# Kernel optimization log

Measured on AMD Instinct MI355X. Metric: run time of the kernel, lower is better.

## Reference

```python
import jax, jax.numpy as jnp
import numpy as np

A = 0.2            # leak rate
SIG_IN = 0.05      # sigma_input_noise
SIG_REC = 0.05     # sigma_rec_noise
N = 256            # n_right_neurons (configs['n_neurons']); left hemi has 2 neurons


def setup_inputs() -> dict:
    key = jax.random.key(0)
    ks = jax.random.split(key, 9)
    B, T = 512, 400

    def nrm(k, shape, scale=1.0):
        return jax.random.normal(k, shape, dtype=jnp.float32) * scale

    xs = nrm(ks[0], (B, T, 2))
    # recurrent weights (asymmetric init, matching torch init_params)
    w_ll = nrm(ks[1], (2, 2), 1.0 / np.sqrt(2))
    b_ll = jnp.zeros((2,), jnp.float32)
    w_rr = nrm(ks[2], (N, N), 1.0 / np.sqrt(N))
    w_rr = w_rr * (3.6 / jnp.sum(jnp.abs(w_rr)))
    b_rr = jnp.zeros((N,), jnp.float32)
    w_lr = nrm(ks[3], (N, 2), 1.0 / np.sqrt(N + 2))   # left -> right
    w_rl = nrm(ks[4], (2, N), 1.0 / np.sqrt(N + 2))   # right -> left
    # input projections (one_hot=True: 2 input channels)
    w_xl = nrm(ks[5], (2, 2))
    w_xr = nrm(ks[6], (N, 2))
    # readout (N+2 -> 1), rescaled so sum(|w|)=3.0
    w_ro = nrm(ks[7], (1, N + 2), 1.0 / np.sqrt(N))
    w_ro = w_ro * (3.0 / jnp.sum(jnp.abs(w_ro)))
    b_ro = jnp.zeros((1,), jnp.float32)
    return {"xs": xs, "w_ll": w_ll, "b_ll": b_ll, "w_rr": w_rr, "b_rr": b_rr,
            "w_lr": w_lr, "w_rl": w_rl, "w_xl": w_xl, "w_xr": w_xr,
            "w_ro": w_ro, "b_ro": b_ro}


def reference(xs, w_ll, b_ll, w_rr, b_rr, w_lr, w_rl, w_xl, w_xr, w_ro, b_ro):
    B, T, _ = xs.shape
    scale = np.sqrt(2.0 / A)
    nk = jax.random.split(jax.random.key(42), 3)
    # input noise (drop masks are all-ones since drop_p=0, amps = 1.0)
    noise_l = scale * SIG_IN * jax.random.normal(nk[0], xs.shape, xs.dtype)
    noise_r = scale * SIG_IN * jax.random.normal(nk[1], xs.shape, xs.dtype)
    x_l = (xs + noise_l) @ w_xl.T                      # (B,T,2)
    x_r = (xs + noise_r) @ w_xr.T                      # (B,T,N)
    x_inj = jnp.concatenate([x_l, x_r], axis=-1)       # (B,T,N+2)
    # recurrent noise, pregenerated for the scan
    rec_noise = scale * SIG_REC * jax.random.normal(nk[2], (T, B, N + 2), xs.dtype)

    def step(h, inp):
        x_t, nz = inp
        hl, hr = h[:, :2], h[:, 2:]
        left = hl @ w_ll.T + hr @ w_rl.T + b_ll        # (B,2)
        right = hl @ w_lr.T + hr @ w_rr.T + b_rr       # (B,N)
        pre = jnp.concatenate([left, right], axis=1) + x_t + nz
        h_new = (1.0 - A) * h + A * jnp.tanh(pre)
        return h_new, h_new

    h0 = jnp.zeros((B, N + 2), xs.dtype)
    _, hs = jax.lax.scan(step, h0, (jnp.swapaxes(x_inj, 0, 1), rec_noise))
    hs = jnp.swapaxes(hs, 0, 1)                        # (B,T,N+2)
    zs = hs @ w_ro.T + b_ro                            # (B,T,1)
    return hs, zs
```

## Files before the change

kernel.cpp:

```cpp
#include <hip/hip_runtime.h>
#include <stdint.h>
#include <stddef.h>


typedef uint32_t u32x4 __attribute__((ext_vector_type(4)));
typedef __fp16   f16x2 __attribute__((ext_vector_type(2)));

#define TF_ROUND(x0, x1, r) { x0 += x1; x1 = ((x1) << (r)) | ((x1) >> (32 - (r))); x1 ^= x0; }

__host__ __device__ inline void tf2x32(uint32_t k0, uint32_t k1, uint32_t x0, uint32_t x1,
                                       uint32_t& o0, uint32_t& o1) {
  uint32_t ks2 = k0 ^ k1 ^ 0x1BD11BDAu;
  x0 += k0; x1 += k1;
  TF_ROUND(x0, x1, 13) TF_ROUND(x0, x1, 15) TF_ROUND(x0, x1, 26) TF_ROUND(x0, x1, 6)
  x0 += k1; x1 += ks2 + 1u;
  TF_ROUND(x0, x1, 17) TF_ROUND(x0, x1, 29) TF_ROUND(x0, x1, 16) TF_ROUND(x0, x1, 24)
  x0 += ks2; x1 += k0 + 2u;
  TF_ROUND(x0, x1, 13) TF_ROUND(x0, x1, 15) TF_ROUND(x0, x1, 26) TF_ROUND(x0, x1, 6)
  x0 += k0; x1 += k1 + 3u;
  TF_ROUND(x0, x1, 17) TF_ROUND(x0, x1, 29) TF_ROUND(x0, x1, 16) TF_ROUND(x0, x1, 24)
  x0 += k1; x1 += ks2 + 4u;
  TF_ROUND(x0, x1, 13) TF_ROUND(x0, x1, 15) TF_ROUND(x0, x1, 26) TF_ROUND(x0, x1, 6)
  x0 += ks2; x1 += k0 + 5u;
  o0 = x0; o1 = x1;
}

__device__ __forceinline__ float jax_erfinv(float x) {
  float w = -log1pf(-x * x);
  float p;
  if (w < 5.0f) {
    w -= 2.5f;
    p = 2.81022636e-08f;
    p = fmaf(p, w, 3.43273939e-07f);
    p = fmaf(p, w, -3.5233877e-06f);
    p = fmaf(p, w, -4.39150654e-06f);
    p = fmaf(p, w, 0.00021858087f);
    p = fmaf(p, w, -0.00125372503f);
    p = fmaf(p, w, -0.00417768164f);
    p = fmaf(p, w, 0.246640727f);
    p = fmaf(p, w, 1.50140941f);
  } else {
    w = sqrtf(w) - 3.0f;
    p = -0.000200214257f;
    p = fmaf(p, w, 0.000100950558f);
    p = fmaf(p, w, 0.00134934322f);
    p = fmaf(p, w, -0.00367342844f);
    p = fmaf(p, w, 0.00573950773f);
    p = fmaf(p, w, -0.0076224613f);
    p = fmaf(p, w, 0.00943887047f);
    p = fmaf(p, w, 1.00167406f);
    p = fmaf(p, w, 2.83297682f);
  }
  return p * x;
}

__device__ __forceinline__ float uni_from_bits(uint32_t bits) {
  float f = __uint_as_float((bits >> 9) | 0x3f800000u) - 1.0f;
  float x = f * 2.0f + (-0.99999994f);
  return fmaxf(-0.99999994f, x);
}

__device__ __forceinline__ float noise_from_bits(uint32_t bits) {
  float n = 1.41421356f * jax_erfinv(uni_from_bits(bits));
  return 0.15811388f * n;
}

__device__ __forceinline__ float my_tanh(float x) {
  float e = __expf(2.0f * x);
  return 1.0f - 2.0f / (e + 1.0f);
}

__device__ __forceinline__ uint32_t packh2(float a, float b) {
  f16x2 h = __builtin_amdgcn_cvt_pkrtz(a, b);
  return __builtin_bit_cast(uint32_t, h);
}

__device__ __forceinline__ void pkfma(uint32_t& acc, uint32_t w, uint32_t h) {
  asm("v_pk_fma_f16 %0, %1, %2, %0" : "+v"(acc) : "v"(w), "v"(h));
}

__device__ __forceinline__ float cvt2f(uint32_t a) {
  f16x2 v = __builtin_bit_cast(f16x2, a);
  return (float)v.x + (float)v.y;
}

__device__ __forceinline__ void step_barrier() {
  asm volatile("s_waitcnt lgkmcnt(0)" ::: "memory");
  __builtin_amdgcn_s_barrier();
}

__device__ __forceinline__ float allred8(float x) {
  int t = __builtin_amdgcn_update_dpp(0, __float_as_int(x), 0xB1, 0xF, 0xF, true);
  x += __int_as_float(t);
  t = __builtin_amdgcn_update_dpp(0, __float_as_int(x), 0x4E, 0xF, 0xF, true);
  x += __int_as_float(t);
  t = __builtin_amdgcn_ds_swizzle(__float_as_int(x), 0x101F);
  x += __int_as_float(t);
  return x;
}

#define PK(kp) (20 * ((kp) >> 4) + ((kp) & 15))

__device__ __forceinline__ float wval(int j, int k,
    const float* w_ll, const float* w_rl, const float* w_lr, const float* w_rr) {
  if (j < 2) return (k < 2) ? w_ll[j * 2 + k] : w_rl[j * 256 + (k - 2)];
  return (k < 2) ? w_lr[(j - 2) * 2 + k] : w_rr[(j - 2) * 256 + (k - 2)];
}

__global__ __launch_bounds__(256) void build_w_kernel(
    const float* __restrict__ w_ll, const float* __restrict__ w_rl,
    const float* __restrict__ w_lr, const float* __restrict__ w_rr,
    uint32_t* __restrict__ Wp, float* __restrict__ Wtail) {
  int i = blockIdx.x * 256 + threadIdx.x;
  if (i < 258 * 128) {
    int j = i >> 7, kp = i & 127;
    float v0 = wval(j, 2 * kp, w_ll, w_rl, w_lr, w_rr);
    float v1 = wval(j, 2 * kp + 1, w_ll, w_rl, w_lr, w_rr);
    Wp[i] = packh2(v0, v1);
  }
  if (i < 516) {
    int j = i >> 1, k = 256 + (i & 1);
    Wtail[i] = wval(j, k, w_ll, w_rl, w_lr, w_rr);
  }
}

__global__ __launch_bounds__(256) void gen_uv_kernel(
    const float* __restrict__ xs, float* __restrict__ u, float* __restrict__ v,
    uint32_t k0a, uint32_t k0b, uint32_t k1a, uint32_t k1b) {
  uint32_t i = blockIdx.x * 256u + threadIdx.x;
  bool isv = i >= 409600u;
  uint32_t e = isv ? i - 409600u : i;
  uint32_t ka = isv ? k1a : k0a;
  uint32_t kb = isv ? k1b : k0b;
  uint32_t o0, o1;
  tf2x32(ka, kb, 0u, e, o0, o1);
  float val = xs[e] + noise_from_bits(o0 ^ o1);
  if (isv) v[e] = val; else u[e] = val;
}

__global__ __launch_bounds__(256) void gen_c_kernel(
    const float* __restrict__ u, const float* __restrict__ v,
    const float* __restrict__ w_xl, const float* __restrict__ w_xr,
    const float* __restrict__ b_ll, const float* __restrict__ b_rr,
    float* __restrict__ C, uint32_t ka, uint32_t kb) {
  uint32_t i = blockIdx.x * 256u + threadIdx.x;
  uint32_t t = i / 132096u;
  uint32_t rem = i - t * 132096u;
  uint32_t b = rem / 258u;
  uint32_t j = rem - b * 258u;
  uint32_t o0, o1;
  tf2x32(ka, kb, 0u, i, o0, o1);
  float nz = noise_from_bits(o0 ^ o1);
  uint32_t bt = (b * 400u + t) * 2u;
  float inj;
  if (j < 2u) {
    float2 uu = *(const float2*)(u + bt);
    inj = w_xl[j * 2u] * uu.x + w_xl[j * 2u + 1u] * uu.y + b_ll[j];
  } else {
    uint32_t jr = j - 2u;
    float2 vv = *(const float2*)(v + bt);
    inj = w_xr[jr * 2u] * vv.x + w_xr[jr * 2u + 1u] * vv.y + b_rr[jr];
  }
  C[(size_t)(b * 400u + t) * 258u + j] = inj + nz;
}

__global__ __launch_bounds__(512, 4) void rnn_scan_kernel(
    const uint32_t* __restrict__ Wp, const float* __restrict__ Wtail,
    float* __restrict__ hsC, const float* __restrict__ w_ro,
    const float* __restrict__ b_ro) {
  __shared__ __align__(16) uint32_t hbp[2][168];
  __shared__ __align__(16) uint32_t wlp[2][168];
  __shared__ __align__(16) float cbuf[8][260];
  __shared__ __align__(16) float sbuf[8][260];
  __shared__ __align__(16) float wrol[260];

  const int tid = threadIdx.x;
  const int ks = tid & 7;
  const int g  = tid >> 3;
  const int j0 = 2 + 4 * g;

  u32x4 wv[4][4];
  float2 wt[4];
#pragma unroll
  for (int r = 0; r < 4; ++r) {
    const uint32_t* p = Wp + (j0 + r) * 128 + 16 * ks;
#pragma unroll
    for (int c = 0; c < 4; ++c) wv[r][c] = *(const u32x4*)(p + 4 * c);
    wt[r] = *(const float2*)(Wtail + (j0 + r) * 2);
  }
  const float bro = b_ro[0];

  if (tid < 256) {
    int row = tid >> 7, kp = tid & 127;
    wlp[row][PK(kp)] = Wp[row * 128 + kp];
  }
  if (tid < 4) {
    int row = tid >> 1;
    wlp[row][160 + (tid & 1)] = __float_as_uint(Wtail[row * 2 + (tid & 1)]);
  }
  if (tid < 258) {
    int jj = (tid < 2) ? (256 + tid) : (tid - 2);
    wrol[jj] = w_ro[tid];
  }
  for (int idx = tid; idx < 336; idx += 512) ((uint32_t*)hbp)[idx] = 0u;

  const float* gC = hsC + (size_t)blockIdx.x * 103200;
  float* gO       = hsC + (size_t)blockIdx.x * 103200;
  float* gZ       = hsC + (size_t)52838400 + (size_t)blockIdx.x * 400;

  for (int idx = tid; idx < 2064; idx += 512) {
    int s = idx / 258, j = idx - 258 * s;
    int jj = (j < 2) ? (256 + j) : (j - 2);
    cbuf[s][jj] = gC[idx];
  }
  __syncthreads();

  float hcur[4] = {0.f, 0.f, 0.f, 0.f};
  float hL0 = 0.f, hL1 = 0.f;

#pragma unroll 1
  for (int cc = 0; cc < 50; ++cc) {
    float creg[5];
    const bool hn = (cc < 49);
    const int nb = (cc + 1) * 2064;
    if (hn) {
#pragma unroll
      for (int q = 0; q < 5; ++q) {
        int idx = tid + 512 * q;
        if (idx < 2064) creg[q] = gC[nb + idx];
      }
    }

#pragma unroll
    for (int s = 0; s < 8; ++s) {
      const int cur = s & 1, nxt = cur ^ 1;

      uint32_t ac0 = 0u, ac1 = 0u, ac2 = 0u, ac3 = 0u;
#pragma unroll
      for (int c = 0; c < 4; ++c) {
        u32x4 hq = *(const u32x4*)&hbp[cur][20 * ks + 4 * c];
        u32x4 w0 = wv[0][c], w1 = wv[1][c], w2 = wv[2][c], w3 = wv[3][c];
        pkfma(ac0, w0.x, hq.x); pkfma(ac0, w0.y, hq.y);
        pkfma(ac0, w0.z, hq.z); pkfma(ac0, w0.w, hq.w);
        pkfma(ac1, w1.x, hq.x); pkfma(ac1, w1.y, hq.y);
        pkfma(ac1, w1.z, hq.z); pkfma(ac1, w1.w, hq.w);
        pkfma(ac2, w2.x, hq.x); pkfma(ac2, w2.y, hq.y);
        pkfma(ac2, w2.z, hq.z); pkfma(ac2, w2.w, hq.w);
        pkfma(ac3, w3.x, hq.x); pkfma(ac3, w3.y, hq.y);
        pkfma(ac3, w3.z, hq.z); pkfma(ac3, w3.w, hq.w);
      }
      float a0 = cvt2f(ac0);
      float a1 = cvt2f(ac1);
      float a2 = cvt2f(ac2);
      float a3 = cvt2f(ac3);

      float l0 = 0.f, l1 = 0.f;
      if (tid < 8) {
        uint32_t lc0 = 0u, lc1 = 0u;
#pragma unroll
        for (int c = 0; c < 4; ++c) {
          u32x4 hq = *(const u32x4*)&hbp[cur][20 * tid + 4 * c];
          u32x4 w0 = *(const u32x4*)&wlp[0][20 * tid + 4 * c];
          u32x4 w1 = *(const u32x4*)&wlp[1][20 * tid + 4 * c];
          pkfma(lc0, w0.x, hq.x); pkfma(lc0, w0.y, hq.y);
          pkfma(lc0, w0.z, hq.z); pkfma(lc0, w0.w, hq.w);
          pkfma(lc1, w1.x, hq.x); pkfma(lc1, w1.y, hq.y);
          pkfma(lc1, w1.z, hq.z); pkfma(lc1, w1.w, hq.w);
        }
        l0 = allred8(cvt2f(lc0));
        l1 = allred8(cvt2f(lc1));
      }

      a0 = allred8(a0); a1 = allred8(a1); a2 = allred8(a2); a3 = allred8(a3);

      const float t0 = __uint_as_float(hbp[cur][160]);
      const float t1 = __uint_as_float(hbp[cur][161]);

      if (ks == 0) {
        float4 cv = *(const float4*)&cbuf[s][4 * g];
        float pre0 = a0 + wt[0].x * t0 + wt[0].y * t1 + cv.x;
        float pre1 = a1 + wt[1].x * t0 + wt[1].y * t1 + cv.y;
        float pre2 = a2 + wt[2].x * t0 + wt[2].y * t1 + cv.z;
        float pre3 = a3 + wt[3].x * t0 + wt[3].y * t1 + cv.w;
        hcur[0] = 0.8f * hcur[0] + 0.2f * my_tanh(pre0);
        hcur[1] = 0.8f * hcur[1] + 0.2f * my_tanh(pre1);
        hcur[2] = 0.8f * hcur[2] + 0.2f * my_tanh(pre2);
        hcur[3] = 0.8f * hcur[3] + 0.2f * my_tanh(pre3);
        uint32_t p01 = packh2(hcur[0], hcur[1]);
        uint32_t p23 = packh2(hcur[2], hcur[3]);
        if (g == 63) {
          hbp[nxt][PK(127)] = p01;
          hbp[nxt][160] = __float_as_uint(hcur[2]);
          hbp[nxt][161] = __float_as_uint(hcur[3]);
        } else {
          hbp[nxt][PK(1 + 2 * g)] = p01;
          hbp[nxt][PK(2 + 2 * g)] = p23;
        }
        *(float4*)&sbuf[s][4 * g] = make_float4(hcur[0], hcur[1], hcur[2], hcur[3]);
      }

      if (tid == 0) {
        float wl0t0 = __uint_as_float(wlp[0][160]);
        float wl0t1 = __uint_as_float(wlp[0][161]);
        float wl1t0 = __uint_as_float(wlp[1][160]);
        float wl1t1 = __uint_as_float(wlp[1][161]);
        float pre0 = l0 + wl0t0 * t0 + wl0t1 * t1 + cbuf[s][256];
        float pre1 = l1 + wl1t0 * t0 + wl1t1 * t1 + cbuf[s][257];
        hL0 = 0.8f * hL0 + 0.2f * my_tanh(pre0);
        hL1 = 0.8f * hL1 + 0.2f * my_tanh(pre1);
        hbp[nxt][0] = packh2(hL0, hL1);
        sbuf[s][256] = hL0;
        sbuf[s][257] = hL1;
      }

      step_barrier();
    }

    const int fb = cc * 2064;
    for (int idx = tid; idx < 2064; idx += 512) {
      int s = idx / 258, j = idx - 258 * s;
      int jj = (j < 2) ? (256 + j) : (j - 2);
      gO[fb + idx] = sbuf[s][jj];
    }

    {
      int w = tid >> 6, lane = tid & 63;
      float zacc = 0.f;
#pragma unroll
      for (int q = 0; q < 5; ++q) {
        int jj = lane + 64 * q;
        if (jj < 258) zacc = fmaf(sbuf[w][jj], wrol[jj], zacc);
      }
#pragma unroll
      for (int m = 32; m >= 1; m >>= 1) zacc += __shfl_xor(zacc, m);
      if (lane == 0) gZ[cc * 8 + w] = zacc + bro;
    }

    if (hn) {
#pragma unroll
      for (int q = 0; q < 5; ++q) {
        int idx = tid + 512 * q;
        if (idx < 2064) {
          int s = idx / 258, j = idx - 258 * s;
          int jj = (j < 2) ? (256 + j) : (j - 2);
          cbuf[s][jj] = creg[q];
        }
      }
    }
    step_barrier();
  }
}

extern "C" void kernel_launch(void* const* d_in, const int* in_sizes, int n_in,
                              void* d_out, int out_size, void* d_ws, size_t ws_size,
                              hipStream_t stream) {
  const float* xs   = (const float*)d_in[0];
  const float* w_ll = (const float*)d_in[1];
  const float* b_ll = (const float*)d_in[2];
  const float* w_rr = (const float*)d_in[3];
  const float* b_rr = (const float*)d_in[4];
  const float* w_lr = (const float*)d_in[5];
  const float* w_rl = (const float*)d_in[6];
  const float* w_xl = (const float*)d_in[7];
  const float* w_xr = (const float*)d_in[8];
  const float* w_ro = (const float*)d_in[9];
  const float* b_ro = (const float*)d_in[10];

  float* hs = (float*)d_out;

  uint32_t* Wp  = (uint32_t*)d_ws;
  float* Wtail  = (float*)(Wp + 33024);
  float* u      = Wtail + 516;
  float* v      = u + 409600;

  uint32_t nk[3][2];
  for (uint32_t i = 0; i < 3; ++i) {
    uint32_t o0, o1;
    tf2x32(0u, 42u, 0u, i, o0, o1);
    nk[i][0] = o0; nk[i][1] = o1;
  }

  build_w_kernel<<<129, 256, 0, stream>>>(w_ll, w_rl, w_lr, w_rr, Wp, Wtail);
  gen_uv_kernel<<<3200, 256, 0, stream>>>(xs, u, v, nk[0][0], nk[0][1], nk[1][0], nk[1][1]);
  gen_c_kernel<<<206400, 256, 0, stream>>>(u, v, w_xl, w_xr, b_ll, b_rr, hs, nk[2][0], nk[2][1]);
  rnn_scan_kernel<<<512, 512, 0, stream>>>(Wp, Wtail, hs, w_ro, b_ro);
}
```

Measured before the change: 1.021 ms.

## Fuse noise and input-injection generation into scan kernel and repartition matvec

Removes the separate gen_uv and gen_c kernels. Each scan block now generates its own input noise into shared memory once, then builds the next 8-step chunk of the drive term (threefry noise plus input projection) in place between chunks. This avoids writing and re-reading the full B*T*258 drive tensor through global memory. The recurrent matvec is also repartitioned: 4 lanes per output pair with 32-wide K slices, a 4-way DPP reduction, weights pinned in registers, and a compacted h buffer layout. The cost is that the threefry and erfinv arithmetic now sits on the serial scan's critical path between chunks, and register pressure goes up.

```diff
diff --git a/kernel.cpp b/kernel.cpp
--- a/kernel.cpp
+++ b/kernel.cpp
@@ -70,11 +70,6 @@
   return 1.0f - 2.0f / (e + 1.0f);
 }
 
-__device__ __forceinline__ uint32_t packh2(float a, float b) {
-  f16x2 h = __builtin_amdgcn_cvt_pkrtz(a, b);
-  return __builtin_bit_cast(uint32_t, h);
-}
-
 __device__ __forceinline__ void pkfma(uint32_t& acc, uint32_t w, uint32_t h) {
   asm("v_pk_fma_f16 %0, %1, %2, %0" : "+v"(acc) : "v"(w), "v"(h));
 }
@@ -84,27 +79,34 @@
   return (float)v.x + (float)v.y;
 }
 
+__device__ __forceinline__ u32x4 pin4(u32x4 x) { asm("" : "+v"(x)); return x; }
+__device__ __forceinline__ float2 pin2(float2 x) { asm("" : "+v"(x)); return x; }
+
 __device__ __forceinline__ void step_barrier() {
   asm volatile("s_waitcnt lgkmcnt(0)" ::: "memory");
   __builtin_amdgcn_s_barrier();
 }
 
-__device__ __forceinline__ float allred8(float x) {
+__device__ __forceinline__ float allred4(float x) {
   int t = __builtin_amdgcn_update_dpp(0, __float_as_int(x), 0xB1, 0xF, 0xF, true);
   x += __int_as_float(t);
   t = __builtin_amdgcn_update_dpp(0, __float_as_int(x), 0x4E, 0xF, 0xF, true);
   x += __int_as_float(t);
-  t = __builtin_amdgcn_ds_swizzle(__float_as_int(x), 0x101F);
-  x += __int_as_float(t);
   return x;
 }
 
-#define PK(kp) (20 * ((kp) >> 4) + ((kp) & 15))
+#define PKQ(acc, wq, hq) { pkfma(acc, (wq).x, (hq).x); pkfma(acc, (wq).y, (hq).y); \
+                           pkfma(acc, (wq).z, (hq).z); pkfma(acc, (wq).w, (hq).w); }
 
 __device__ __forceinline__ float wval(int j, int k,
     const float* w_ll, const float* w_rl, const float* w_lr, const float* w_rr) {
   if (j < 2) return (k < 2) ? w_ll[j * 2 + k] : w_rl[j * 256 + (k - 2)];
   return (k < 2) ? w_lr[(j - 2) * 2 + k] : w_rr[(j - 2) * 256 + (k - 2)];
+}
+
+__device__ __forceinline__ uint32_t packh2(float a, float b) {
+  f16x2 h = __builtin_amdgcn_cvt_pkrtz(a, b);
+  return __builtin_bit_cast(uint32_t, h);
 }
 
 __global__ __launch_bounds__(256) void build_w_kernel(
@@ -124,203 +126,180 @@
   }
 }
 
-__global__ __launch_bounds__(256) void gen_uv_kernel(
-    const float* __restrict__ xs, float* __restrict__ u, float* __restrict__ v,
-    uint32_t k0a, uint32_t k0b, uint32_t k1a, uint32_t k1b) {
-  uint32_t i = blockIdx.x * 256u + threadIdx.x;
-  bool isv = i >= 409600u;
-  uint32_t e = isv ? i - 409600u : i;
-  uint32_t ka = isv ? k1a : k0a;
-  uint32_t kb = isv ? k1b : k0b;
-  uint32_t o0, o1;
-  tf2x32(ka, kb, 0u, e, o0, o1);
-  float val = xs[e] + noise_from_bits(o0 ^ o1);
-  if (isv) v[e] = val; else u[e] = val;
-}
-
-__global__ __launch_bounds__(256) void gen_c_kernel(
-    const float* __restrict__ u, const float* __restrict__ v,
+__global__ __launch_bounds__(512, 4) void rnn_scan_kernel(
+    const uint32_t* __restrict__ Wp, const float* __restrict__ Wtail,
+    float* __restrict__ hsC,
+    const float* __restrict__ w_ro, const float* __restrict__ b_ro,
+    const float* __restrict__ xs,
     const float* __restrict__ w_xl, const float* __restrict__ w_xr,
     const float* __restrict__ b_ll, const float* __restrict__ b_rr,
-    float* __restrict__ C, uint32_t ka, uint32_t kb) {
-  uint32_t i = blockIdx.x * 256u + threadIdx.x;
-  uint32_t t = i / 132096u;
-  uint32_t rem = i - t * 132096u;
-  uint32_t b = rem / 258u;
-  uint32_t j = rem - b * 258u;
-  uint32_t o0, o1;
-  tf2x32(ka, kb, 0u, i, o0, o1);
-  float nz = noise_from_bits(o0 ^ o1);
-  uint32_t bt = (b * 400u + t) * 2u;
-  float inj;
-  if (j < 2u) {
-    float2 uu = *(const float2*)(u + bt);
-    inj = w_xl[j * 2u] * uu.x + w_xl[j * 2u + 1u] * uu.y + b_ll[j];
-  } else {
-    uint32_t jr = j - 2u;
-    float2 vv = *(const float2*)(v + bt);
-    inj = w_xr[jr * 2u] * vv.x + w_xr[jr * 2u + 1u] * vv.y + b_rr[jr];
-  }
-  C[(size_t)(b * 400u + t) * 258u + j] = inj + nz;
-}
-
-__global__ __launch_bounds__(512, 4) void rnn_scan_kernel(
-    const uint32_t* __restrict__ Wp, const float* __restrict__ Wtail,
-    float* __restrict__ hsC, const float* __restrict__ w_ro,
-    const float* __restrict__ b_ro) {
-  __shared__ __align__(16) uint32_t hbp[2][168];
-  __shared__ __align__(16) uint32_t wlp[2][168];
+    uint32_t k0a, uint32_t k0b, uint32_t k1a, uint32_t k1b,
+    uint32_t k2a, uint32_t k2b) {
+  __shared__ __align__(16) uint32_t hbp[2][132];
+  __shared__ __align__(16) uint32_t wlp[2][132];
   __shared__ __align__(16) float cbuf[8][260];
   __shared__ __align__(16) float sbuf[8][260];
-  __shared__ __align__(16) float wrol[260];
+  __shared__ float wrol[260];
+  __shared__ float uvb[400][4];
+  __shared__ float wxr[256][2];
+  __shared__ float brr[256];
+  __shared__ float wxl[4];
+  __shared__ float bll[2];
 
   const int tid = threadIdx.x;
-  const int ks = tid & 7;
-  const int g  = tid >> 3;
-  const int j0 = 2 + 4 * g;
-
-  u32x4 wv[4][4];
-  float2 wt[4];
-#pragma unroll
-  for (int r = 0; r < 4; ++r) {
-    const uint32_t* p = Wp + (j0 + r) * 128 + 16 * ks;
-#pragma unroll
-    for (int c = 0; c < 4; ++c) wv[r][c] = *(const u32x4*)(p + 4 * c);
-    wt[r] = *(const float2*)(Wtail + (j0 + r) * 2);
-  }
+  const int brow = blockIdx.x;
+  const int ks = tid & 3;
+  const int g  = tid >> 2;
+  const int j0 = 2 + 2 * g;
+  const int lrow = (tid >= 4) ? 1 : 0;
+
+  u32x4 wr0[8], wr1[8];
+  {
+    const uint32_t* p0 = Wp + (size_t)j0 * 128 + 32 * ks;
+    const uint32_t* p1 = p0 + 128;
+#pragma unroll
+    for (int c = 0; c < 8; ++c) {
+      wr0[c] = pin4(*(const u32x4*)(p0 + 4 * c));
+      wr1[c] = pin4(*(const u32x4*)(p1 + 4 * c));
+    }
+  }
+  const float2 wt0 = pin2(*(const float2*)(Wtail + (size_t)j0 * 2));
+  const float2 wt1 = pin2(*(const float2*)(Wtail + (size_t)j0 * 2 + 2));
   const float bro = b_ro[0];
 
   if (tid < 256) {
+    wxr[tid][0] = w_xr[2 * tid];
+    wxr[tid][1] = w_xr[2 * tid + 1];
+    brr[tid] = b_rr[tid];
     int row = tid >> 7, kp = tid & 127;
-    wlp[row][PK(kp)] = Wp[row * 128 + kp];
-  }
-  if (tid < 4) {
-    int row = tid >> 1;
-    wlp[row][160 + (tid & 1)] = __float_as_uint(Wtail[row * 2 + (tid & 1)]);
-  }
-  if (tid < 258) {
-    int jj = (tid < 2) ? (256 + tid) : (tid - 2);
-    wrol[jj] = w_ro[tid];
-  }
-  for (int idx = tid; idx < 336; idx += 512) ((uint32_t*)hbp)[idx] = 0u;
-
-  const float* gC = hsC + (size_t)blockIdx.x * 103200;
-  float* gO       = hsC + (size_t)blockIdx.x * 103200;
-  float* gZ       = hsC + (size_t)52838400 + (size_t)blockIdx.x * 400;
-
-  for (int idx = tid; idx < 2064; idx += 512) {
-    int s = idx / 258, j = idx - 258 * s;
-    int jj = (j < 2) ? (256 + j) : (j - 2);
-    cbuf[s][jj] = gC[idx];
+    wlp[row][kp] = Wp[row * 128 + kp];
+  }
+  if (tid < 4) wxl[tid] = w_xl[tid];
+  if (tid < 2) bll[tid] = b_ll[tid];
+  if (tid < 4) { int row = tid >> 1; wlp[row][128 + (tid & 1)] = __float_as_uint(Wtail[row * 2 + (tid & 1)]); }
+  if (tid < 258) { int jj = (tid < 2) ? (256 + tid) : (tid - 2); wrol[jj] = w_ro[tid]; }
+  for (int i2 = tid; i2 < 264; i2 += 512) ((uint32_t*)hbp)[i2] = 0u;
+
+  for (int idx = tid; idx < 1600; idx += 512) {
+    int t = idx >> 2, q = idx & 3;
+    uint32_t e = (uint32_t)(brow * 800 + t * 2 + (q & 1));
+    uint32_t o0, o1;
+    if (q < 2) tf2x32(k0a, k0b, 0u, e, o0, o1);
+    else       tf2x32(k1a, k1b, 0u, e, o0, o1);
+    uvb[t][q] = xs[e] + noise_from_bits(o0 ^ o1);
   }
   __syncthreads();
 
-  float hcur[4] = {0.f, 0.f, 0.f, 0.f};
-  float hL0 = 0.f, hL1 = 0.f;
+  auto gen_cbuf = [&](int cc) {
+#pragma unroll
+    for (int q = 0; q < 5; ++q) {
+      int idx = tid + 512 * q;
+      if (idx < 2064) {
+        int s = idx / 258;
+        int j = idx - 258 * s;
+        int t = cc * 8 + s;
+        uint32_t o0, o1;
+        tf2x32(k2a, k2b, 0u, (uint32_t)(t * 132096 + brow * 258 + j), o0, o1);
+        float nz = noise_from_bits(o0 ^ o1);
+        float inj;
+        int jj;
+        if (j < 2) {
+          inj = wxl[2 * j] * uvb[t][0] + wxl[2 * j + 1] * uvb[t][1] + bll[j];
+          jj = 256 + j;
+        } else {
+          int jr = j - 2;
+          inj = wxr[jr][0] * uvb[t][2] + wxr[jr][1] * uvb[t][3] + brr[jr];
+          jj = jr;
+        }
+        cbuf[s][jj] = inj + nz;
+      }
+    }
+  };
+
+  gen_cbuf(0);
+  __syncthreads();
+
+  float hcur = 0.f;
+  float hL = 0.f;
+
+  float* gO = hsC + (size_t)brow * 103200;
+  float* gZ = hsC + (size_t)52838400 + (size_t)brow * 400;
 
 #pragma unroll 1
   for (int cc = 0; cc < 50; ++cc) {
-    float creg[5];
-    const bool hn = (cc < 49);
-    const int nb = (cc + 1) * 2064;
-    if (hn) {
-#pragma unroll
-      for (int q = 0; q < 5; ++q) {
-        int idx = tid + 512 * q;
-        if (idx < 2064) creg[q] = gC[nb + idx];
-      }
-    }
-
 #pragma unroll
     for (int s = 0; s < 8; ++s) {
       const int cur = s & 1, nxt = cur ^ 1;
 
-      uint32_t ac0 = 0u, ac1 = 0u, ac2 = 0u, ac3 = 0u;
-#pragma unroll
-      for (int c = 0; c < 4; ++c) {
-        u32x4 hq = *(const u32x4*)&hbp[cur][20 * ks + 4 * c];
-        u32x4 w0 = wv[0][c], w1 = wv[1][c], w2 = wv[2][c], w3 = wv[3][c];
-        pkfma(ac0, w0.x, hq.x); pkfma(ac0, w0.y, hq.y);
-        pkfma(ac0, w0.z, hq.z); pkfma(ac0, w0.w, hq.w);
-        pkfma(ac1, w1.x, hq.x); pkfma(ac1, w1.y, hq.y);
-        pkfma(ac1, w1.z, hq.z); pkfma(ac1, w1.w, hq.w);
-        pkfma(ac2, w2.x, hq.x); pkfma(ac2, w2.y, hq.y);
-        pkfma(ac2, w2.z, hq.z); pkfma(ac2, w2.w, hq.w);
-        pkfma(ac3, w3.x, hq.x); pkfma(ac3, w3.y, hq.y);
-        pkfma(ac3, w3.z, hq.z); pkfma(ac3, w3.w, hq.w);
-      }
-      float a0 = cvt2f(ac0);
-      float a1 = cvt2f(ac1);
-      float a2 = cvt2f(ac2);
-      float a3 = cvt2f(ac3);
-
-      float l0 = 0.f, l1 = 0.f;
+      float t0 = __uint_as_float(hbp[cur][128]);
+      float t1 = __uint_as_float(hbp[cur][129]);
+      float2 cv = *(const float2*)&cbuf[s][2 * g];
+
+      const uint32_t* hb = &hbp[cur][32 * ks];
+      uint32_t acA0 = 0u, acA1 = 0u, acB0 = 0u, acB1 = 0u, lcA = 0u, lcB = 0u;
+      {
+        u32x4 h0 = *(const u32x4*)(hb + 0),  h1 = *(const u32x4*)(hb + 4),
+              h2 = *(const u32x4*)(hb + 8),  h3 = *(const u32x4*)(hb + 12);
+        PKQ(acA0, wr0[0], h0) PKQ(acA0, wr0[1], h1) PKQ(acA0, wr0[2], h2) PKQ(acA0, wr0[3], h3)
+        PKQ(acA1, wr1[0], h0) PKQ(acA1, wr1[1], h1) PKQ(acA1, wr1[2], h2) PKQ(acA1, wr1[3], h3)
+        if (tid < 8) {
+          const uint32_t* wl = &wlp[lrow][32 * ks];
+          u32x4 w0 = *(const u32x4*)(wl + 0), w1 = *(const u32x4*)(wl + 4),
+                w2 = *(const u32x4*)(wl + 8), w3 = *(const u32x4*)(wl + 12);
+          PKQ(lcA, w0, h0) PKQ(lcA, w1, h1) PKQ(lcA, w2, h2) PKQ(lcA, w3, h3)
+        }
+      }
+      {
+        u32x4 h0 = *(const u32x4*)(hb + 16), h1 = *(const u32x4*)(hb + 20),
+              h2 = *(const u32x4*)(hb + 24), h3 = *(const u32x4*)(hb + 28);
+        PKQ(acB0, wr0[4], h0) PKQ(acB0, wr0[5], h1) PKQ(acB0, wr0[6], h2) PKQ(acB0, wr0[7], h3)
+        PKQ(acB1, wr1[4], h0) PKQ(acB1, wr1[5], h1) PKQ(acB1, wr1[6], h2) PKQ(acB1, wr1[7], h3)
+        if (tid < 8) {
+          const uint32_t* wl = &wlp[lrow][32 * ks + 16];
+          u32x4 w0 = *(const u32x4*)(wl + 0), w1 = *(const u32x4*)(wl + 4),
+                w2 = *(const u32x4*)(wl + 8), w3 = *(const u32x4*)(wl + 12);
+          PKQ(lcB, w0, h0) PKQ(lcB, w1, h1) PKQ(lcB, w2, h2) PKQ(lcB, w3, h3)
+        }
+      }
+
+      float a0 = allred4(cvt2f(acA0) + cvt2f(acB0));
+      float a1 = allred4(cvt2f(acA1) + cvt2f(acB1));
+
+      if (ks < 2) {
+        float a   = ks ? a1 : a0;
+        float2 wt = ks ? wt1 : wt0;
+        float cvx = ks ? cv.y : cv.x;
+        float pre = a + wt.x * t0 + wt.y * t1 + cvx;
+        hcur = 0.8f * hcur + 0.2f * my_tanh(pre);
+        sbuf[s][2 * g + ks] = hcur;
+        if (g == 127) hbp[nxt][128 + ks] = __float_as_uint(hcur);
+        else *(__fp16*)((char*)&hbp[nxt][0] + 4 * (1 + g) + 2 * ks) = (__fp16)hcur;
+      }
+
       if (tid < 8) {
-        uint32_t lc0 = 0u, lc1 = 0u;
-#pragma unroll
-        for (int c = 0; c < 4; ++c) {
-          u32x4 hq = *(const u32x4*)&hbp[cur][20 * tid + 4 * c];
-          u32x4 w0 = *(const u32x4*)&wlp[0][20 * tid + 4 * c];
-          u32x4 w1 = *(const u32x4*)&wlp[1][20 * tid + 4 * c];
-          pkfma(lc0, w0.x, hq.x); pkfma(lc0, w0.y, hq.y);
-          pkfma(lc0, w0.z, hq.z); pkfma(lc0, w0.w, hq.w);
-          pkfma(lc1, w1.x, hq.x); pkfma(lc1, w1.y, hq.y);
-          pkfma(lc1, w1.z, hq.z); pkfma(lc1, w1.w, hq.w);
+        float l = allred4(cvt2f(lcA) + cvt2f(lcB));
+        if ((tid & 3) == 0) {
+          float wlt0 = __uint_as_float(wlp[lrow][128]);
+          float wlt1 = __uint_as_float(wlp[lrow][129]);
+          float pre = l + wlt0 * t0 + wlt1 * t1 + cbuf[s][256 + lrow];
+          hL = 0.8f * hL + 0.2f * my_tanh(pre);
+          sbuf[s][256 + lrow] = hL;
+          *(__fp16*)((char*)&hbp[nxt][0] + 2 * lrow) = (__fp16)hL;
         }
-        l0 = allred8(cvt2f(lc0));
-        l1 = allred8(cvt2f(lc1));
-      }
-
-      a0 = allred8(a0); a1 = allred8(a1); a2 = allred8(a2); a3 = allred8(a3);
-
-      const float t0 = __uint_as_float(hbp[cur][160]);
-      const float t1 = __uint_as_float(hbp[cur][161]);
-
-      if (ks == 0) {
-        float4 cv = *(const float4*)&cbuf[s][4 * g];
-        float pre0 = a0 + wt[0].x * t0 + wt[0].y * t1 + cv.x;
-        float pre1 = a1 + wt[1].x * t0 + wt[1].y * t1 + cv.y;
-        float pre2 = a2 + wt[2].x * t0 + wt[2].y * t1 + cv.z;
-        float pre3 = a3 + wt[3].x * t0 + wt[3].y * t1 + cv.w;
-        hcur[0] = 0.8f * hcur[0] + 0.2f * my_tanh(pre0);
-        hcur[1] = 0.8f * hcur[1] + 0.2f * my_tanh(pre1);
-        hcur[2] = 0.8f * hcur[2] + 0.2f * my_tanh(pre2);
-        hcur[3] = 0.8f * hcur[3] + 0.2f * my_tanh(pre3);
-        uint32_t p01 = packh2(hcur[0], hcur[1]);
-        uint32_t p23 = packh2(hcur[2], hcur[3]);
-        if (g == 63) {
-          hbp[nxt][PK(127)] = p01;
-          hbp[nxt][160] = __float_as_uint(hcur[2]);
-          hbp[nxt][161] = __float_as_uint(hcur[3]);
-        } else {
-          hbp[nxt][PK(1 + 2 * g)] = p01;
-          hbp[nxt][PK(2 + 2 * g)] = p23;
-        }
-        *(float4*)&sbuf[s][4 * g] = make_float4(hcur[0], hcur[1], hcur[2], hcur[3]);
-      }
-
-      if (tid == 0) {
-        float wl0t0 = __uint_as_float(wlp[0][160]);
-        float wl0t1 = __uint_as_float(wlp[0][161]);
-        float wl1t0 = __uint_as_float(wlp[1][160]);
-        float wl1t1 = __uint_as_float(wlp[1][161]);
-        float pre0 = l0 + wl0t0 * t0 + wl0t1 * t1 + cbuf[s][256];
-        float pre1 = l1 + wl1t0 * t0 + wl1t1 * t1 + cbuf[s][257];
-        hL0 = 0.8f * hL0 + 0.2f * my_tanh(pre0);
-        hL1 = 0.8f * hL1 + 0.2f * my_tanh(pre1);
-        hbp[nxt][0] = packh2(hL0, hL1);
-        sbuf[s][256] = hL0;
-        sbuf[s][257] = hL1;
       }
 
       step_barrier();
     }
 
     const int fb = cc * 2064;
-    for (int idx = tid; idx < 2064; idx += 512) {
-      int s = idx / 258, j = idx - 258 * s;
-      int jj = (j < 2) ? (256 + j) : (j - 2);
-      gO[fb + idx] = sbuf[s][jj];
+#pragma unroll
+    for (int q = 0; q < 5; ++q) {
+      int idx = tid + 512 * q;
+      if (idx < 2064) {
+        int s = idx / 258, j = idx - 258 * s;
+        int jj = (j < 2) ? (256 + j) : (j - 2);
+        gO[fb + idx] = sbuf[s][jj];
+      }
     }
 
     {
@@ -336,17 +315,7 @@
       if (lane == 0) gZ[cc * 8 + w] = zacc + bro;
     }
 
-    if (hn) {
-#pragma unroll
-      for (int q = 0; q < 5; ++q) {
-        int idx = tid + 512 * q;
-        if (idx < 2064) {
-          int s = idx / 258, j = idx - 258 * s;
-          int jj = (j < 2) ? (256 + j) : (j - 2);
-          cbuf[s][jj] = creg[q];
-        }
-      }
-    }
+    if (cc < 49) gen_cbuf(cc + 1);
     step_barrier();
   }
 }
@@ -370,8 +339,6 @@
 
   uint32_t* Wp  = (uint32_t*)d_ws;
   float* Wtail  = (float*)(Wp + 33024);
-  float* u      = Wtail + 516;
-  float* v      = u + 409600;
 
   uint32_t nk[3][2];
   for (uint32_t i = 0; i < 3; ++i) {
@@ -381,7 +348,8 @@
   }
 
   build_w_kernel<<<129, 256, 0, stream>>>(w_ll, w_rl, w_lr, w_rr, Wp, Wtail);
-  gen_uv_kernel<<<3200, 256, 0, stream>>>(xs, u, v, nk[0][0], nk[0][1], nk[1][0], nk[1][1]);
-  gen_c_kernel<<<206400, 256, 0, stream>>>(u, v, w_xl, w_xr, b_ll, b_rr, hs, nk[2][0], nk[2][1]);
-  rnn_scan_kernel<<<512, 512, 0, stream>>>(Wp, Wtail, hs, w_ro, b_ro);
-}
+  rnn_scan_kernel<<<512, 512, 0, stream>>>(Wp, Wtail, hs, w_ro, b_ro, xs,
+                                           w_xl, w_xr, b_ll, b_rr,
+                                           nk[0][0], nk[0][1], nk[1][0], nk[1][1],
+                                           nk[2][0], nk[2][1]);
+}
```

New measurement: 1.557 ms. 1.52x slower.

## Fuse noise and input-injection generation into the RNN scan kernel

Applied to the files above, without the earlier changes.

Removes the separate gen_uv and gen_c kernels, so each scan block now generates its own threefry noise and input projection on chip, one 8-step chunk at a time, between chunks. This drops the full-size write and read of the injected-input tensor through global memory, along with two kernel launches. In exchange, the threefry hashing sits on the serial scan's critical path between chunks instead of overlapping with the global prefetch. Shared memory also grows to hold the per-row noisy inputs and the projection weights, and empty asm statements pin the weight registers.

```diff
diff --git a/kernel.cpp b/kernel.cpp
--- a/kernel.cpp
+++ b/kernel.cpp
@@ -124,57 +124,28 @@
   }
 }
 
-__global__ __launch_bounds__(256) void gen_uv_kernel(
-    const float* __restrict__ xs, float* __restrict__ u, float* __restrict__ v,
-    uint32_t k0a, uint32_t k0b, uint32_t k1a, uint32_t k1b) {
-  uint32_t i = blockIdx.x * 256u + threadIdx.x;
-  bool isv = i >= 409600u;
-  uint32_t e = isv ? i - 409600u : i;
-  uint32_t ka = isv ? k1a : k0a;
-  uint32_t kb = isv ? k1b : k0b;
-  uint32_t o0, o1;
-  tf2x32(ka, kb, 0u, e, o0, o1);
-  float val = xs[e] + noise_from_bits(o0 ^ o1);
-  if (isv) v[e] = val; else u[e] = val;
-}
-
-__global__ __launch_bounds__(256) void gen_c_kernel(
-    const float* __restrict__ u, const float* __restrict__ v,
+__global__ __launch_bounds__(512, 4) void rnn_scan_kernel(
+    const uint32_t* __restrict__ Wp, const float* __restrict__ Wtail,
+    float* __restrict__ hsC,
+    const float* __restrict__ w_ro, const float* __restrict__ b_ro,
+    const float* __restrict__ xs,
     const float* __restrict__ w_xl, const float* __restrict__ w_xr,
     const float* __restrict__ b_ll, const float* __restrict__ b_rr,
-    float* __restrict__ C, uint32_t ka, uint32_t kb) {
-  uint32_t i = blockIdx.x * 256u + threadIdx.x;
-  uint32_t t = i / 132096u;
-  uint32_t rem = i - t * 132096u;
-  uint32_t b = rem / 258u;
-  uint32_t j = rem - b * 258u;
-  uint32_t o0, o1;
-  tf2x32(ka, kb, 0u, i, o0, o1);
-  float nz = noise_from_bits(o0 ^ o1);
-  uint32_t bt = (b * 400u + t) * 2u;
-  float inj;
-  if (j < 2u) {
-    float2 uu = *(const float2*)(u + bt);
-    inj = w_xl[j * 2u] * uu.x + w_xl[j * 2u + 1u] * uu.y + b_ll[j];
-  } else {
-    uint32_t jr = j - 2u;
-    float2 vv = *(const float2*)(v + bt);
-    inj = w_xr[jr * 2u] * vv.x + w_xr[jr * 2u + 1u] * vv.y + b_rr[jr];
-  }
-  C[(size_t)(b * 400u + t) * 258u + j] = inj + nz;
-}
-
-__global__ __launch_bounds__(512, 4) void rnn_scan_kernel(
-    const uint32_t* __restrict__ Wp, const float* __restrict__ Wtail,
-    float* __restrict__ hsC, const float* __restrict__ w_ro,
-    const float* __restrict__ b_ro) {
+    uint32_t k0a, uint32_t k0b, uint32_t k1a, uint32_t k1b,
+    uint32_t k2a, uint32_t k2b) {
   __shared__ __align__(16) uint32_t hbp[2][168];
   __shared__ __align__(16) uint32_t wlp[2][168];
   __shared__ __align__(16) float cbuf[8][260];
   __shared__ __align__(16) float sbuf[8][260];
-  __shared__ __align__(16) float wrol[260];
+  __shared__ float wrol[260];
+  __shared__ float uvb[400][4];
+  __shared__ float wxr[256][2];
+  __shared__ float brr[256];
+  __shared__ float wxl[4];
+  __shared__ float bll[2];
 
   const int tid = threadIdx.x;
+  const int brow = blockIdx.x;
   const int ks = tid & 7;
   const int g  = tid >> 3;
   const int j0 = 2 + 4 * g;
@@ -188,49 +159,80 @@
     for (int c = 0; c < 4; ++c) wv[r][c] = *(const u32x4*)(p + 4 * c);
     wt[r] = *(const float2*)(Wtail + (j0 + r) * 2);
   }
+#pragma unroll
+  for (int r = 0; r < 4; ++r) {
+#pragma unroll
+    for (int c = 0; c < 4; ++c) asm volatile("" : "+v"(wv[r][c]));
+    asm volatile("" : "+v"(wt[r]));
+  }
   const float bro = b_ro[0];
 
   if (tid < 256) {
     int row = tid >> 7, kp = tid & 127;
     wlp[row][PK(kp)] = Wp[row * 128 + kp];
+    wxr[tid][0] = w_xr[2 * tid];
+    wxr[tid][1] = w_xr[2 * tid + 1];
+    brr[tid] = b_rr[tid];
   }
   if (tid < 4) {
     int row = tid >> 1;
     wlp[row][160 + (tid & 1)] = __float_as_uint(Wtail[row * 2 + (tid & 1)]);
-  }
+    wxl[tid] = w_xl[tid];
+  }
+  if (tid < 2) bll[tid] = b_ll[tid];
   if (tid < 258) {
     int jj = (tid < 2) ? (256 + tid) : (tid - 2);
     wrol[jj] = w_ro[tid];
   }
   for (int idx = tid; idx < 336; idx += 512) ((uint32_t*)hbp)[idx] = 0u;
 
-  const float* gC = hsC + (size_t)blockIdx.x * 103200;
-  float* gO       = hsC + (size_t)blockIdx.x * 103200;
-  float* gZ       = hsC + (size_t)52838400 + (size_t)blockIdx.x * 400;
-
-  for (int idx = tid; idx < 2064; idx += 512) {
-    int s = idx / 258, j = idx - 258 * s;
-    int jj = (j < 2) ? (256 + j) : (j - 2);
-    cbuf[s][jj] = gC[idx];
-  }
+  for (int idx = tid; idx < 1600; idx += 512) {
+    int t = idx >> 2, q = idx & 3;
+    uint32_t e = (uint32_t)(brow * 800 + t * 2 + (q & 1));
+    uint32_t o0, o1;
+    if (q < 2) tf2x32(k0a, k0b, 0u, e, o0, o1);
+    else       tf2x32(k1a, k1b, 0u, e, o0, o1);
+    uvb[t][q] = xs[e] + noise_from_bits(o0 ^ o1);
+  }
+  __syncthreads();
+
+  auto gen_cbuf = [&](int cc) {
+#pragma unroll
+    for (int q = 0; q < 5; ++q) {
+      int idx = tid + 512 * q;
+      if (idx < 2064) {
+        int s = idx / 258;
+        int j = idx - 258 * s;
+        int t = cc * 8 + s;
+        uint32_t o0, o1;
+        tf2x32(k2a, k2b, 0u, (uint32_t)(t * 132096 + brow * 258 + j), o0, o1);
+        float nz = noise_from_bits(o0 ^ o1);
+        float inj;
+        int jj;
+        if (j < 2) {
+          inj = wxl[2 * j] * uvb[t][0] + wxl[2 * j + 1] * uvb[t][1] + bll[j];
+          jj = 256 + j;
+        } else {
+          int jr = j - 2;
+          inj = wxr[jr][0] * uvb[t][2] + wxr[jr][1] * uvb[t][3] + brr[jr];
+          jj = jr;
+        }
+        cbuf[s][jj] = inj + nz;
+      }
+    }
+  };
+
+  gen_cbuf(0);
   __syncthreads();
 
   float hcur[4] = {0.f, 0.f, 0.f, 0.f};
   float hL0 = 0.f, hL1 = 0.f;
 
+  float* gO = hsC + (size_t)brow * 103200;
+  float* gZ = hsC + (size_t)52838400 + (size_t)brow * 400;
+
 #pragma unroll 1
   for (int cc = 0; cc < 50; ++cc) {
-    float creg[5];
-    const bool hn = (cc < 49);
-    const int nb = (cc + 1) * 2064;
-    if (hn) {
-#pragma unroll
-      for (int q = 0; q < 5; ++q) {
-        int idx = tid + 512 * q;
-        if (idx < 2064) creg[q] = gC[nb + idx];
-      }
-    }
-
 #pragma unroll
     for (int s = 0; s < 8; ++s) {
       const int cur = s & 1, nxt = cur ^ 1;
@@ -317,10 +319,14 @@
     }
 
     const int fb = cc * 2064;
-    for (int idx = tid; idx < 2064; idx += 512) {
-      int s = idx / 258, j = idx - 258 * s;
-      int jj = (j < 2) ? (256 + j) : (j - 2);
-      gO[fb + idx] = sbuf[s][jj];
+#pragma unroll
+    for (int q = 0; q < 5; ++q) {
+      int idx = tid + 512 * q;
+      if (idx < 2064) {
+        int s = idx / 258, j = idx - 258 * s;
+        int jj = (j < 2) ? (256 + j) : (j - 2);
+        gO[fb + idx] = sbuf[s][jj];
+      }
     }
 
     {
@@ -336,17 +342,7 @@
       if (lane == 0) gZ[cc * 8 + w] = zacc + bro;
     }
 
-    if (hn) {
-#pragma unroll
-      for (int q = 0; q < 5; ++q) {
-        int idx = tid + 512 * q;
-        if (idx < 2064) {
-          int s = idx / 258, j = idx - 258 * s;
-          int jj = (j < 2) ? (256 + j) : (j - 2);
-          cbuf[s][jj] = creg[q];
-        }
-      }
-    }
+    if (cc < 49) gen_cbuf(cc + 1);
     step_barrier();
   }
 }
@@ -370,8 +366,6 @@
 
   uint32_t* Wp  = (uint32_t*)d_ws;
   float* Wtail  = (float*)(Wp + 33024);
-  float* u      = Wtail + 516;
-  float* v      = u + 409600;
 
   uint32_t nk[3][2];
   for (uint32_t i = 0; i < 3; ++i) {
@@ -381,7 +375,8 @@
   }
 
   build_w_kernel<<<129, 256, 0, stream>>>(w_ll, w_rl, w_lr, w_rr, Wp, Wtail);
-  gen_uv_kernel<<<3200, 256, 0, stream>>>(xs, u, v, nk[0][0], nk[0][1], nk[1][0], nk[1][1]);
-  gen_c_kernel<<<206400, 256, 0, stream>>>(u, v, w_xl, w_xr, b_ll, b_rr, hs, nk[2][0], nk[2][1]);
-  rnn_scan_kernel<<<512, 512, 0, stream>>>(Wp, Wtail, hs, w_ro, b_ro);
-}
+  rnn_scan_kernel<<<512, 512, 0, stream>>>(Wp, Wtail, hs, w_ro, b_ro, xs,
+                                           w_xl, w_xr, b_ll, b_rr,
+                                           nk[0][0], nk[0][1], nk[1][0], nk[1][1],
+                                           nk[2][0], nk[2][1]);
+}
```

After: 1.671 ms. +63.7%, slower.

## Compute recurrent matvec with MFMA 16x16x32 f16 instead of packed FMA plus DPP reductions

Applied to the files above, without the earlier changes.

The per-step recurrent matrix-vector product moves from v_pk_fma_f16 accumulation followed by 8-lane DPP all-reductions to MFMA f32_16x16x32_f16 instructions. Each wave keeps its 32-row slice of the weights resident in registers as B fragments and reads the broadcast hidden vector from LDS as the A operand. Only the lanes holding the first output row apply the tanh update. The shared-memory layout is also simplified to natural ordering with no padding or permutation, and weight loads are pinned with inline asm. This removes the cross-lane reductions and raises per-step math throughput. In exchange, 15 of 16 MFMA rows do wasted work, and the step still depends on MFMA latency plus single-lane fp16 LDS writes.

```diff
diff --git a/kernel.cpp b/kernel.cpp
--- a/kernel.cpp
+++ b/kernel.cpp
@@ -5,6 +5,8 @@
 
 typedef uint32_t u32x4 __attribute__((ext_vector_type(4)));
 typedef __fp16   f16x2 __attribute__((ext_vector_type(2)));
+typedef __fp16   f16x8 __attribute__((ext_vector_type(8)));
+typedef float    f32x4 __attribute__((ext_vector_type(4)));
 
 #define TF_ROUND(x0, x1, r) { x0 += x1; x1 = ((x1) << (r)) | ((x1) >> (32 - (r))); x1 ^= x0; }
 
@@ -84,6 +86,13 @@
   return (float)v.x + (float)v.y;
 }
 
+__device__ __forceinline__ u32x4 vload_pin(const uint32_t* p) {
+  u32x4 r;
+  asm volatile("global_load_dwordx4 %0, %1, off\n\ts_waitcnt vmcnt(0)"
+               : "=v"(r) : "v"(p) : "memory");
+  return r;
+}
+
 __device__ __forceinline__ void step_barrier() {
   asm volatile("s_waitcnt lgkmcnt(0)" ::: "memory");
   __builtin_amdgcn_s_barrier();
@@ -98,8 +107,6 @@
   x += __int_as_float(t);
   return x;
 }
-
-#define PK(kp) (20 * ((kp) >> 4) + ((kp) & 15))
 
 __device__ __forceinline__ float wval(int j, int k,
     const float* w_ll, const float* w_rl, const float* w_lr, const float* w_rr) {
@@ -168,41 +175,37 @@
     const uint32_t* __restrict__ Wp, const float* __restrict__ Wtail,
     float* __restrict__ hsC, const float* __restrict__ w_ro,
     const float* __restrict__ b_ro) {
-  __shared__ __align__(16) uint32_t hbp[2][168];
-  __shared__ __align__(16) uint32_t wlp[2][168];
+  __shared__ __align__(16) uint32_t hA[2][132];
+  __shared__ float htail[2][2];
+  __shared__ __align__(16) uint32_t wlp[2][128];
+  __shared__ __align__(16) float wtl[520];
   __shared__ __align__(16) float cbuf[8][260];
   __shared__ __align__(16) float sbuf[8][260];
-  __shared__ __align__(16) float wrol[260];
-
-  const int tid = threadIdx.x;
-  const int ks = tid & 7;
-  const int g  = tid >> 3;
-  const int j0 = 2 + 4 * g;
-
-  u32x4 wv[4][4];
-  float2 wt[4];
-#pragma unroll
-  for (int r = 0; r < 4; ++r) {
-    const uint32_t* p = Wp + (j0 + r) * 128 + 16 * ks;
-#pragma unroll
-    for (int c = 0; c < 4; ++c) wv[r][c] = *(const u32x4*)(p + 4 * c);
-    wt[r] = *(const float2*)(Wtail + (j0 + r) * 2);
+  __shared__ float wrol[260];
+
+  const int tid  = threadIdx.x;
+  const int lane = tid & 63;
+  const int wv   = tid >> 6;
+  const int lq   = lane >> 4;
+
+  u32x4 B0[8], B1[8];
+  {
+    const int j0 = 32 * wv + 2 + (lane & 15);
+    const uint32_t* base0 = Wp + (size_t)j0 * 128 + 4 * lq;
+    const uint32_t* base1 = base0 + 16 * 128;
+#pragma unroll
+    for (int kt = 0; kt < 8; ++kt) {
+      B0[kt] = vload_pin(base0 + 16 * kt);
+      B1[kt] = vload_pin(base1 + 16 * kt);
+    }
   }
   const float bro = b_ro[0];
 
-  if (tid < 256) {
-    int row = tid >> 7, kp = tid & 127;
-    wlp[row][PK(kp)] = Wp[row * 128 + kp];
-  }
-  if (tid < 4) {
-    int row = tid >> 1;
-    wlp[row][160 + (tid & 1)] = __float_as_uint(Wtail[row * 2 + (tid & 1)]);
-  }
-  if (tid < 258) {
-    int jj = (tid < 2) ? (256 + tid) : (tid - 2);
-    wrol[jj] = w_ro[tid];
-  }
-  for (int idx = tid; idx < 336; idx += 512) ((uint32_t*)hbp)[idx] = 0u;
+  if (tid < 256) wlp[tid >> 7][tid & 127] = Wp[(size_t)(tid >> 7) * 128 + (tid & 127)];
+  if (tid < 258) wrol[tid] = w_ro[tid];
+  for (int i = tid; i < 516; i += 512) wtl[i] = Wtail[i];
+  for (int i = tid; i < 264; i += 512) ((uint32_t*)hA)[i] = 0u;
+  if (tid < 4) ((float*)htail)[tid] = 0.f;
 
   const float* gC = hsC + (size_t)blockIdx.x * 103200;
   float* gO       = hsC + (size_t)blockIdx.x * 103200;
@@ -210,12 +213,11 @@
 
   for (int idx = tid; idx < 2064; idx += 512) {
     int s = idx / 258, j = idx - 258 * s;
-    int jj = (j < 2) ? (256 + j) : (j - 2);
-    cbuf[s][jj] = gC[idx];
+    cbuf[s][j] = gC[idx];
   }
   __syncthreads();
 
-  float hcur[4] = {0.f, 0.f, 0.f, 0.f};
+  float hp0 = 0.f, hp1 = 0.f;
   float hL0 = 0.f, hL1 = 0.f;
 
 #pragma unroll 1
@@ -235,33 +237,25 @@
     for (int s = 0; s < 8; ++s) {
       const int cur = s & 1, nxt = cur ^ 1;
 
-      uint32_t ac0 = 0u, ac1 = 0u, ac2 = 0u, ac3 = 0u;
-#pragma unroll
-      for (int c = 0; c < 4; ++c) {
-        u32x4 hq = *(const u32x4*)&hbp[cur][20 * ks + 4 * c];
-        u32x4 w0 = wv[0][c], w1 = wv[1][c], w2 = wv[2][c], w3 = wv[3][c];
-        pkfma(ac0, w0.x, hq.x); pkfma(ac0, w0.y, hq.y);
-        pkfma(ac0, w0.z, hq.z); pkfma(ac0, w0.w, hq.w);
-        pkfma(ac1, w1.x, hq.x); pkfma(ac1, w1.y, hq.y);
-        pkfma(ac1, w1.z, hq.z); pkfma(ac1, w1.w, hq.w);
-        pkfma(ac2, w2.x, hq.x); pkfma(ac2, w2.y, hq.y);
-        pkfma(ac2, w2.z, hq.z); pkfma(ac2, w2.w, hq.w);
-        pkfma(ac3, w3.x, hq.x); pkfma(ac3, w3.y, hq.y);
-        pkfma(ac3, w3.z, hq.z); pkfma(ac3, w3.w, hq.w);
-      }
-      float a0 = cvt2f(ac0);
-      float a1 = cvt2f(ac1);
-      float a2 = cvt2f(ac2);
-      float a3 = cvt2f(ac3);
+      f32x4 d0 = {0.f, 0.f, 0.f, 0.f};
+      f32x4 d1 = {0.f, 0.f, 0.f, 0.f};
+      const uint32_t* ha = hA[cur];
+#pragma unroll
+      for (int kt = 0; kt < 8; ++kt) {
+        u32x4 av = *(const u32x4*)(ha + 16 * kt + 4 * lq);
+        f16x8 af = __builtin_bit_cast(f16x8, av);
+        d0 = __builtin_amdgcn_mfma_f32_16x16x32_f16(af, __builtin_bit_cast(f16x8, B0[kt]), d0, 0, 0, 0);
+        d1 = __builtin_amdgcn_mfma_f32_16x16x32_f16(af, __builtin_bit_cast(f16x8, B1[kt]), d1, 0, 0, 0);
+      }
 
       float l0 = 0.f, l1 = 0.f;
       if (tid < 8) {
         uint32_t lc0 = 0u, lc1 = 0u;
 #pragma unroll
         for (int c = 0; c < 4; ++c) {
-          u32x4 hq = *(const u32x4*)&hbp[cur][20 * tid + 4 * c];
-          u32x4 w0 = *(const u32x4*)&wlp[0][20 * tid + 4 * c];
-          u32x4 w1 = *(const u32x4*)&wlp[1][20 * tid + 4 * c];
+          u32x4 hq = *(const u32x4*)&hA[cur][16 * tid + 4 * c];
+          u32x4 w0 = *(const u32x4*)&wlp[0][16 * tid + 4 * c];
+          u32x4 w1 = *(const u32x4*)&wlp[1][16 * tid + 4 * c];
           pkfma(lc0, w0.x, hq.x); pkfma(lc0, w0.y, hq.y);
           pkfma(lc0, w0.z, hq.z); pkfma(lc0, w0.w, hq.w);
           pkfma(lc1, w1.x, hq.x); pkfma(lc1, w1.y, hq.y);
@@ -271,69 +265,62 @@
         l1 = allred8(cvt2f(lc1));
       }
 
-      a0 = allred8(a0); a1 = allred8(a1); a2 = allred8(a2); a3 = allred8(a3);
-
-      const float t0 = __uint_as_float(hbp[cur][160]);
-      const float t1 = __uint_as_float(hbp[cur][161]);
-
-      if (ks == 0) {
-        float4 cv = *(const float4*)&cbuf[s][4 * g];
-        float pre0 = a0 + wt[0].x * t0 + wt[0].y * t1 + cv.x;
-        float pre1 = a1 + wt[1].x * t0 + wt[1].y * t1 + cv.y;
-        float pre2 = a2 + wt[2].x * t0 + wt[2].y * t1 + cv.z;
-        float pre3 = a3 + wt[3].x * t0 + wt[3].y * t1 + cv.w;
-        hcur[0] = 0.8f * hcur[0] + 0.2f * my_tanh(pre0);
-        hcur[1] = 0.8f * hcur[1] + 0.2f * my_tanh(pre1);
-        hcur[2] = 0.8f * hcur[2] + 0.2f * my_tanh(pre2);
-        hcur[3] = 0.8f * hcur[3] + 0.2f * my_tanh(pre3);
-        uint32_t p01 = packh2(hcur[0], hcur[1]);
-        uint32_t p23 = packh2(hcur[2], hcur[3]);
-        if (g == 63) {
-          hbp[nxt][PK(127)] = p01;
-          hbp[nxt][160] = __float_as_uint(hcur[2]);
-          hbp[nxt][161] = __float_as_uint(hcur[3]);
-        } else {
-          hbp[nxt][PK(1 + 2 * g)] = p01;
-          hbp[nxt][PK(2 + 2 * g)] = p23;
+      const float t0v = htail[cur][0];
+      const float t1v = htail[cur][1];
+
+      if (lane < 16) {
+        {
+          int j = 32 * wv + 2 + lane;
+          float2 wt2 = *(const float2*)&wtl[2 * j];
+          float pre = d0.x + wt2.x * t0v + wt2.y * t1v + cbuf[s][j];
+          hp0 = 0.8f * hp0 + 0.2f * my_tanh(pre);
+          sbuf[s][j] = hp0;
+          ((__fp16*)hA[nxt])[j] = (__fp16)hp0;
         }
-        *(float4*)&sbuf[s][4 * g] = make_float4(hcur[0], hcur[1], hcur[2], hcur[3]);
+        {
+          int j = 32 * wv + 18 + lane;
+          float2 wt2 = *(const float2*)&wtl[2 * j];
+          float pre = d1.x + wt2.x * t0v + wt2.y * t1v + cbuf[s][j];
+          hp1 = 0.8f * hp1 + 0.2f * my_tanh(pre);
+          sbuf[s][j] = hp1;
+          if (j < 256) ((__fp16*)hA[nxt])[j] = (__fp16)hp1;
+          else         htail[nxt][j - 256] = hp1;
+        }
       }
 
       if (tid == 0) {
-        float wl0t0 = __uint_as_float(wlp[0][160]);
-        float wl0t1 = __uint_as_float(wlp[0][161]);
-        float wl1t0 = __uint_as_float(wlp[1][160]);
-        float wl1t1 = __uint_as_float(wlp[1][161]);
-        float pre0 = l0 + wl0t0 * t0 + wl0t1 * t1 + cbuf[s][256];
-        float pre1 = l1 + wl1t0 * t0 + wl1t1 * t1 + cbuf[s][257];
+        float pre0 = l0 + wtl[0] * t0v + wtl[1] * t1v + cbuf[s][0];
+        float pre1 = l1 + wtl[2] * t0v + wtl[3] * t1v + cbuf[s][1];
         hL0 = 0.8f * hL0 + 0.2f * my_tanh(pre0);
         hL1 = 0.8f * hL1 + 0.2f * my_tanh(pre1);
-        hbp[nxt][0] = packh2(hL0, hL1);
-        sbuf[s][256] = hL0;
-        sbuf[s][257] = hL1;
+        hA[nxt][0] = packh2(hL0, hL1);
+        sbuf[s][0] = hL0;
+        sbuf[s][1] = hL1;
       }
 
       step_barrier();
     }
 
     const int fb = cc * 2064;
-    for (int idx = tid; idx < 2064; idx += 512) {
-      int s = idx / 258, j = idx - 258 * s;
-      int jj = (j < 2) ? (256 + j) : (j - 2);
-      gO[fb + idx] = sbuf[s][jj];
+#pragma unroll
+    for (int q = 0; q < 5; ++q) {
+      int idx = tid + 512 * q;
+      if (idx < 2064) {
+        int s = idx / 258, j = idx - 258 * s;
+        gO[fb + idx] = sbuf[s][j];
+      }
     }
 
     {
-      int w = tid >> 6, lane = tid & 63;
       float zacc = 0.f;
 #pragma unroll
       for (int q = 0; q < 5; ++q) {
         int jj = lane + 64 * q;
-        if (jj < 258) zacc = fmaf(sbuf[w][jj], wrol[jj], zacc);
+        if (jj < 258) zacc = fmaf(sbuf[wv][jj], wrol[jj], zacc);
       }
 #pragma unroll
       for (int m = 32; m >= 1; m >>= 1) zacc += __shfl_xor(zacc, m);
-      if (lane == 0) gZ[cc * 8 + w] = zacc + bro;
+      if (lane == 0) gZ[cc * 8 + wv] = zacc + bro;
     }
 
     if (hn) {
@@ -342,8 +329,7 @@
         int idx = tid + 512 * q;
         if (idx < 2064) {
           int s = idx / 258, j = idx - 258 * s;
-          int jj = (j < 2) ? (256 + j) : (j - 2);
-          cbuf[s][jj] = creg[q];
+          cbuf[s][j] = creg[q];
         }
       }
     }
```

Measured after the change: 910.7 us. -10.8%, faster.
